# Performance work log

Measured on AMD Instinct MI355X. Metric: run time of the kernel, lower is better.

## Reference

```python
import jax, jax.numpy as jnp
import numpy as np

B, N, E, S, HOPS, OD = 32, 325, 64, 12, 3, 1


def setup_inputs() -> dict:
    key = jax.random.key(0)
    ks = jax.random.split(key, 16)
    rn = lambda k, sh: jax.random.normal(k, sh, dtype=jnp.float32)
    return {
        "hidden": rn(ks[0], (B, N, E)),
        "supports": jax.random.uniform(ks[1], (2, N, N), dtype=jnp.float32),
        "target": rn(ks[2], (B, S, N, OD)),
        "memory": rn(ks[3], (HOPS + 1, B, N, E)),
        "nodevec1": rn(ks[4], (N, E)),
        "nodevec2": rn(ks[5], (N, E)),
        "gru_w_ih": rn(ks[6], (3 * E, OD)) * 0.1,
        "gru_w_hh": rn(ks[7], (3 * E, E)) * 0.1,
        "gru_b_ih": rn(ks[8], (3 * E,)) * 0.1,
        "gru_b_hh": rn(ks[9], (3 * E,)) * 0.1,
        "sent_w": rn(ks[10], (HOPS, E, E)) * 0.1,  # sentinel Linear (no bias), stored pre-transposed
        "bn_gamma": jnp.ones((HOPS, N), dtype=jnp.float32),
        "bn_beta": jnp.zeros((HOPS, N), dtype=jnp.float32),
        "gconv_w": rn(ks[11], (HOPS, 7 * E, E)) * 0.05,  # order*support_len+1 = 7 chunks
        "gconv_b": rn(ks[12], (HOPS, E)) * 0.05,
        "out_w": rn(ks[13], (E, OD)) * 0.1,
        "out_b": rn(ks[14], (OD,)) * 0.1,
    }


def _bn(x, gamma, beta, eps=1e-5):
    # nn.BatchNorm1d(num_nodes) on (B, N, E): channel dim is N, stats over (B, E) (training-mode batch stats)
    mean = x.mean(axis=(0, 2), keepdims=True)
    var = x.var(axis=(0, 2), keepdims=True)
    return (x - mean) / jnp.sqrt(var + eps) * gamma[None, :, None] + beta[None, :, None]


def _gconv(x, sup_list, score, W, b):
    # order=2, support_len=3 -> 1 + 2*3 = 7 concatenated chunks, then Linear(7E -> E)
    outs = [x]
    for adj in sup_list:
        x1 = jnp.einsum('nm,bme->bne', adj, x)
        outs.append(jnp.einsum('bnm,bme->bne', score, x1))
        x2 = jnp.einsum('nm,bme->bne', adj, x1)
        outs.append(jnp.einsum('bnm,bme->bne', score, x2))
    return jnp.concatenate(outs, axis=-1) @ W + b


def reference(hidden, supports, target, memory, nodevec1, nodevec2,
              gru_w_ih, gru_w_hh, gru_b_ih, gru_b_hh, sent_w,
              bn_gamma, bn_beta, gconv_w, gconv_b, out_w, out_b):
    Bn, Nn, Ee = hidden.shape
    scale = Ee ** 0.5
    adp = jax.nn.softmax(jax.nn.relu(nodevec1 @ nodevec2.T), axis=-1)
    sup_list = [supports[0], supports[1], adp]

    def step(carry, _):
        h, prev = carry  # h: (B,N,E), prev: (B,N,OD) previous prediction (zeros at t=0)
        gi = prev.reshape(Bn * Nn, -1) @ gru_w_ih.T + gru_b_ih
        gh = h.reshape(Bn * Nn, Ee) @ gru_w_hh.T + gru_b_hh
        i_r, i_z, i_n = jnp.split(gi, 3, axis=-1)
        h_r, h_z, h_n = jnp.split(gh, 3, axis=-1)
        r = jax.nn.sigmoid(i_r + h_r)
        z = jax.nn.sigmoid(i_z + h_z)
        n = jnp.tanh(i_n + r * h_n)
        h_new = ((1.0 - z) * n + z * h.reshape(Bn * Nn, Ee)).reshape(Bn, Nn, Ee)
        u = h_new
        sents, mems = [], []
        for hop in range(HOPS):
            key_m = memory[hop]  # (B,N,E)
            energy = jnp.einsum('bne,bme->bnm', u, key_m) / scale  # (B,N,N)
            sent = jnp.sum(u * (key_m @ sent_w[hop]), axis=-1) / scale  # (B,N)
            sents.append(sent)
            score = jax.nn.softmax(energy, axis=-1)
            o = _bn(_gconv(memory[hop + 1], sup_list, score, gconv_w[hop], gconv_b[hop]),
                    bn_gamma[hop], bn_beta[hop])
            mems.append(o)
            u = u + o
        sents = jnp.stack(sents, axis=-1)   # (B,N,hops)
        mems = jnp.stack(mems, axis=-2)     # (B,N,hops,E)
        # NOTE: original code weights with RAW sentinel energies, not sentinel_score (dead code) -- kept faithful
        out = jnp.sum(sents[..., None] * mems, axis=-2) @ out_w + out_b  # (B,N,OD)
        return (h_new, out), out

    init_out = jnp.zeros((Bn, Nn, OD), dtype=hidden.dtype)
    _, outs = jax.lax.scan(step, (hidden, init_out), None, length=S)  # (S,B,N,OD)
    return jnp.transpose(outs, (1, 0, 2, 3))  # (B,S,N,OD)
```

## Files before the change

kernel.cpp:

```cpp
#include <hip/hip_runtime.h>

constexpr int B = 32, N = 325, E = 64, S = 12, HOPS = 3;
constexpr int BN  = B * N;
constexpr int BNE = B * N * E;
constexpr int RT  = 16;
constexpr int NRT = (N + RT - 1) / RT;
constexpr int EP  = E + 4;
constexpr int NP  = 328;
constexpr int PBSTR = 360;
constexpr float SCALE_INV = 0.125f;

typedef __attribute__((ext_vector_type(8))) short short8v;
typedef __attribute__((ext_vector_type(4))) float f32x4;

__device__ inline short f2bf(float f) {
  unsigned x = __builtin_bit_cast(unsigned, f);
  return (short)((x + 0x7FFFu + ((x >> 16) & 1u)) >> 16);
}
__device__ inline float bf2f(short h) {
  unsigned x = ((unsigned)(unsigned short)h) << 16;
  return __builtin_bit_cast(float, x);
}

__global__ __launch_bounds__(256) void adp_kernel(const float* __restrict__ nv1,
                                                  const float* __restrict__ nv2,
                                                  float* __restrict__ adp) {
  int n = blockIdx.x;
  __shared__ float row[E];
  __shared__ float buf[N];
  __shared__ float red[256];
  int tid = threadIdx.x;
  if (tid < E) row[tid] = nv1[n * E + tid];
  __syncthreads();
  float lmax = -1e30f;
  for (int m = tid; m < N; m += 256) {
    const float* v2 = nv2 + (size_t)m * E;
    float s = 0.f;
#pragma unroll
    for (int e = 0; e < E; ++e) s += row[e] * v2[e];
    s = fmaxf(s, 0.f);
    buf[m] = s;
    lmax = fmaxf(lmax, s);
  }
  red[tid] = lmax;
  __syncthreads();
  for (int off = 128; off > 0; off >>= 1) {
    if (tid < off) red[tid] = fmaxf(red[tid], red[tid + off]);
    __syncthreads();
  }
  float mx = red[0];
  __syncthreads();
  float lsum = 0.f;
  for (int m = tid; m < N; m += 256) {
    float ev = expf(buf[m] - mx);
    buf[m] = ev;
    lsum += ev;
  }
  red[tid] = lsum;
  __syncthreads();
  for (int off = 128; off > 0; off >>= 1) {
    if (tid < off) red[tid] += red[tid + off];
    __syncthreads();
  }
  float inv = 1.f / red[0];
  for (int m = tid; m < N; m += 256) adp[(size_t)n * N + m] = buf[m] * inv;
}

__device__ inline void rowmm_body(const float* __restrict__ in, const float* __restrict__ W,
                                  const float* __restrict__ bias, float* __restrict__ out,
                                  int accum, int blk, int nblk) {
  __shared__ float Wl[E][E + 1];
  __shared__ float rbuf[4][4][E];
  int tid = threadIdx.x, w = tid >> 6, l = tid & 63;
  for (int idx = tid; idx < E * E; idx += 256) Wl[idx >> 6][idx & 63] = W[idx];
  __syncthreads();
  float bv = bias ? bias[l] : 0.f;
  constexpr int NG = BN / 16;
  for (int g = blk; g < NG; g += nblk) {
    int base = g * 16 + w * 4;
#pragma unroll
    for (int rr = 0; rr < 4; ++rr) rbuf[w][rr][l] = in[(size_t)(base + rr) * E + l];
    float acc[4];
#pragma unroll
    for (int rr = 0; rr < 4; ++rr)
      acc[rr] = accum ? out[(size_t)(base + rr) * E + l] : bv;
#pragma unroll
    for (int k = 0; k < 16; ++k) {
      float w0 = Wl[4 * k][l], w1 = Wl[4 * k + 1][l], w2 = Wl[4 * k + 2][l], w3 = Wl[4 * k + 3][l];
#pragma unroll
      for (int rr = 0; rr < 4; ++rr) {
        float4 rv = *(const float4*)&rbuf[w][rr][4 * k];
        acc[rr] += rv.x * w0 + rv.y * w1 + rv.z * w2 + rv.w * w3;
      }
    }
#pragma unroll
    for (int rr = 0; rr < 4; ++rr) out[(size_t)(base + rr) * E + l] = acc[rr];
  }
}

__global__ __launch_bounds__(256) void rowmmA_kernel(const float* __restrict__ memory,
                                                     const float* __restrict__ sent_w,
                                                     const float* __restrict__ gw,
                                                     const float* __restrict__ gb,
                                                     float* __restrict__ kms,
                                                     float* __restrict__ C0) {
  int c = blockIdx.x / 112, blk = blockIdx.x % 112;
  const float *in, *W, *bias;
  float* out;
  if (c < 3) {
    in = memory + (size_t)c * BNE; W = sent_w + (size_t)c * E * E; bias = nullptr;
    out = kms + (size_t)c * BNE;
  } else {
    int h = c - 3;
    in = memory + (size_t)(h + 1) * BNE; W = gw + (size_t)h * 7 * E * E; bias = gb + h * E;
    out = C0 + (size_t)h * BNE;
  }
  rowmm_body(in, W, bias, out, 0, blk, 112);
}

__global__ __launch_bounds__(256) void rowmmZ_kernel(const float* __restrict__ tbase,
                                                     const float* __restrict__ gw,
                                                     int chunk, float* __restrict__ Zb,
                                                     int accum) {
  int h = blockIdx.x / 224, blk = blockIdx.x % 224;
  rowmm_body(tbase + (size_t)h * BNE, gw + (size_t)h * 7 * E * E + (size_t)chunk * E * E,
             nullptr, Zb + (size_t)h * BNE, accum, blk, 224);
}

__global__ __launch_bounds__(256) void bmmB_kernel(const float* __restrict__ A,
                                                   const float* __restrict__ Xbase,
                                                   float* __restrict__ outBase) {
  int c = blockIdx.x / (B * NRT), rem = blockIdx.x % (B * NRT);
  int b = rem / NRT, rt = rem % NRT;
  const float* X = Xbase + (size_t)c * BNE;
  float* out = outBase + (size_t)c * BNE;
  int n0 = rt * RT, nrows = min(RT, N - n0);
  __shared__ float Ar[RT][NP];
  __shared__ float tile[64][EP];
  int tid = threadIdx.x, w = tid >> 6, l = tid & 63;
  for (int r = w; r < RT; r += 4)
    for (int m = l; m < NP; m += 64)
      Ar[r][m] = (r < nrows && m < N) ? A[(size_t)(n0 + r) * N + m] : 0.f;
  int ti = tid >> 2, c0 = (tid & 3) * 16;
  float acc[4] = {0.f, 0.f, 0.f, 0.f};
  for (int mt = 0; mt < 6; ++mt) {
    int m0 = mt * 64, mv = min(64, N - m0);
    __syncthreads();
    {
      float4 z0, z1, z2, z3;
      if (ti < mv) {
        const float4* src = (const float4*)(X + ((size_t)b * N + m0 + ti) * E + c0);
        z0 = src[0]; z1 = src[1]; z2 = src[2]; z3 = src[3];
      } else {
        z0 = z1 = z2 = z3 = make_float4(0.f, 0.f, 0.f, 0.f);
      }
      float4* dst = (float4*)&tile[ti][c0];
      dst[0] = z0; dst[1] = z1; dst[2] = z2; dst[3] = z3;
    }
    __syncthreads();
    int jmax = (mv + 3) >> 2;
#pragma unroll 4
    for (int j = 0; j < jmax; ++j) {
      float t0 = tile[4 * j][l], t1 = tile[4 * j + 1][l];
      float t2 = tile[4 * j + 2][l], t3 = tile[4 * j + 3][l];
#pragma unroll
      for (int rr = 0; rr < 4; ++rr) {
        float4 p = *(const float4*)&Ar[w * 4 + rr][m0 + 4 * j];
        acc[rr] += p.x * t0 + p.y * t1 + p.z * t2 + p.w * t3;
      }
    }
  }
#pragma unroll
  for (int rr = 0; rr < 4; ++rr) {
    int r = w * 4 + rr;
    if (r < nrows) out[((size_t)b * N + n0 + r) * E + l] = acc[rr];
  }
}

__global__ __launch_bounds__(128) void kpack_kernel(const float* __restrict__ memory,
                                                    short* __restrict__ kp) {
  int idx = blockIdx.x;
  int ct = idx % 21, hb = idx / 21;
  int tid = threadIdx.x, ks = tid >> 6, l = tid & 63;
  int m = ct * 16 + (l & 15);
  int e0 = ks * 32 + (l >> 4) * 8;
  short8v hi, lo;
  if (m < N) {
    const float* p = memory + ((size_t)hb * N + m) * E + e0;
#pragma unroll
    for (int j = 0; j < 8; ++j) {
      float f = p[j];
      short h = f2bf(f);
      hi[j] = h;
      lo[j] = f2bf(f - bf2f(h));
    }
  } else {
#pragma unroll
    for (int j = 0; j < 8; ++j) { hi[j] = 0; lo[j] = 0; }
  }
  size_t base = ((size_t)idx * 2 + ks) * 1024 + (size_t)l * 8;
  *(short8v*)(kp + base) = hi;
  *(short8v*)(kp + base + 512) = lo;
}

__global__ __launch_bounds__(64) void zpack_kernel(const float* __restrict__ Zb,
                                                   short* __restrict__ zp) {
  int idx = blockIdx.x;
  int et = idx & 3, hb = idx >> 2;
  int l = threadIdx.x;
  int e = et * 16 + (l & 15);
  int mbase = (l >> 4) * 8;
  const float* Zp = Zb + (size_t)hb * N * E;
  for (int ks = 0; ks < 11; ++ks) {
    short8v hi, lo;
#pragma unroll
    for (int j = 0; j < 8; ++j) {
      int m = ks * 32 + mbase + j;
      float f = (m < N) ? Zp[(size_t)m * E + e] : 0.f;
      short h = f2bf(f);
      hi[j] = h;
      lo[j] = f2bf(f - bf2f(h));
    }
    size_t base = ((size_t)idx * 11 + ks) * 1024 + (size_t)l * 8;
    *(short8v*)(zp + base) = hi;
    *(short8v*)(zp + base + 512) = lo;
  }
}

__global__ __launch_bounds__(512) void attn_kernel(
    const float* __restrict__ uPrev, const float* __restrict__ gprePrev,
    const float* __restrict__ statsPrev, const float* __restrict__ gammaPrev,
    const float* __restrict__ betaPrev, const float* __restrict__ outw,
    float* __restrict__ uOut, float* __restrict__ owPrev,
    const float* __restrict__ kms, const short* __restrict__ kp,
    const short* __restrict__ zp, const float* __restrict__ C0,
    float* __restrict__ gpre, float* __restrict__ statsCur,
    float* __restrict__ sent) {
  int b = blockIdx.x / 11, rt = blockIdx.x % 11;
  int n0 = rt * 32, nrows = min(32, N - n0);
  int tid = threadIdx.x, w = tid >> 6, l = tid & 63;
  __shared__ float uT[32][68];
  __shared__ short pb[32][PBSTR];
  __shared__ float rowred[32][8];
  __shared__ float rmax[32];
  __shared__ float rsinv[32];
  size_t rowbase = (size_t)b * N + n0;
  int g = l >> 4;

  for (int idx = tid; idx < 32 * (PBSTR - 336); idx += 512) {
    int r = idx / (PBSTR - 336), c = idx - r * (PBSTR - 336);
    pb[r][336 + c] = 0;
  }
#pragma unroll
  for (int rr = 0; rr < 4; ++rr) {
    int r = w * 4 + rr;
    if (r < nrows) {
      size_t gi = (rowbase + r) * E + l;
      float uv;
      if (gprePrev) {
        int n = n0 + r;
        float m = statsPrev[n] * (1.f / 2048.f);
        float var = statsPrev[N + n] * (1.f / 2048.f) - m * m;
        float rstd = rsqrtf(var + 1e-5f);
        float o = (gprePrev[gi] - m) * rstd * gammaPrev[n] + betaPrev[n];
        uv = uPrev[gi] + o;
        if (uOut) uOut[gi] = uv;
        float tt = o * outw[l];
#pragma unroll
        for (int off = 32; off; off >>= 1) tt += __shfl_xor(tt, off);
        if (l == 0) owPrev[rowbase + r] = tt;
      } else {
        uv = uPrev[gi];
      }
      uT[r][l] = uv;
    } else {
      uT[r][l] = 0.f;
    }
  }
  __syncthreads();
#pragma unroll
  for (int rr = 0; rr < 4; ++rr) {
    int r = w * 4 + rr;
    if (r < nrows) {
      float v = uT[r][l] * kms[(rowbase + r) * E + l];
#pragma unroll
      for (int off = 32; off; off >>= 1) v += __shfl_xor(v, off);
      if (l == 0) sent[rowbase + r] = v * SCALE_INV;
    }
  }
  short8v ah[2][2], al[2][2];
  {
    int arow = l & 15, ak = g * 8;
#pragma unroll
    for (int mt = 0; mt < 2; ++mt)
#pragma unroll
      for (int ks = 0; ks < 2; ++ks) {
        const float* p = &uT[mt * 16 + arow][ks * 32 + ak];
        short8v h, lo;
#pragma unroll
        for (int j = 0; j < 8; ++j) {
          float f = p[j];
          short hh = f2bf(f);
          h[j] = hh;
          lo[j] = f2bf(f - bf2f(hh));
        }
        ah[mt][ks] = h; al[mt][ks] = lo;
      }
  }
  const short8v* kpb = (const short8v*)(kp + (size_t)b * 21 * 2048);
  f32x4 acc0[3], acc1[3];
#pragma unroll
  for (int i = 0; i < 3; ++i) {
    acc0[i] = (f32x4){0.f, 0.f, 0.f, 0.f};
    acc1[i] = (f32x4){0.f, 0.f, 0.f, 0.f};
    int ct = w + 8 * i;
    if (ct < 21) {
      short8v bh0 = kpb[(ct * 4 + 0) * 64 + l];
      short8v bl0 = kpb[(ct * 4 + 1) * 64 + l];
      short8v bh1 = kpb[(ct * 4 + 2) * 64 + l];
      short8v bl1 = kpb[(ct * 4 + 3) * 64 + l];
      f32x4 a0 = acc0[i], a1 = acc1[i];
      a0 = __builtin_amdgcn_mfma_f32_16x16x32_bf16(ah[0][0], bh0, a0, 0, 0, 0);
      a0 = __builtin_amdgcn_mfma_f32_16x16x32_bf16(ah[0][0], bl0, a0, 0, 0, 0);
      a0 = __builtin_amdgcn_mfma_f32_16x16x32_bf16(al[0][0], bh0, a0, 0, 0, 0);
      a0 = __builtin_amdgcn_mfma_f32_16x16x32_bf16(ah[0][1], bh1, a0, 0, 0, 0);
      a0 = __builtin_amdgcn_mfma_f32_16x16x32_bf16(ah[0][1], bl1, a0, 0, 0, 0);
      a0 = __builtin_amdgcn_mfma_f32_16x16x32_bf16(al[0][1], bh1, a0, 0, 0, 0);
      a1 = __builtin_amdgcn_mfma_f32_16x16x32_bf16(ah[1][0], bh0, a1, 0, 0, 0);
      a1 = __builtin_amdgcn_mfma_f32_16x16x32_bf16(ah[1][0], bl0, a1, 0, 0, 0);
      a1 = __builtin_amdgcn_mfma_f32_16x16x32_bf16(al[1][0], bh0, a1, 0, 0, 0);
      a1 = __builtin_amdgcn_mfma_f32_16x16x32_bf16(ah[1][1], bh1, a1, 0, 0, 0);
      a1 = __builtin_amdgcn_mfma_f32_16x16x32_bf16(ah[1][1], bl1, a1, 0, 0, 0);
      a1 = __builtin_amdgcn_mfma_f32_16x16x32_bf16(al[1][1], bh1, a1, 0, 0, 0);
      acc0[i] = a0; acc1[i] = a1;
    }
  }
  {
    float m0[4], m1[4];
#pragma unroll
    for (int r = 0; r < 4; ++r) {
      float a = -1e30f, c = -1e30f;
#pragma unroll
      for (int i = 0; i < 3; ++i)
        if (w + 8 * i < 21) { a = fmaxf(a, acc0[i][r]); c = fmaxf(c, acc1[i][r]); }
#pragma unroll
      for (int off = 1; off < 16; off <<= 1) {
        a = fmaxf(a, __shfl_xor(a, off));
        c = fmaxf(c, __shfl_xor(c, off));
      }
      m0[r] = a; m1[r] = c;
    }
    if ((l & 15) == 0) {
#pragma unroll
      for (int r = 0; r < 4; ++r) {
        rowred[g * 4 + r][w] = m0[r];
        rowred[16 + g * 4 + r][w] = m1[r];
      }
    }
  }
  __syncthreads();
  if (tid < 32) {
    float a = rowred[tid][0];
#pragma unroll
    for (int j = 1; j < 8; ++j) a = fmaxf(a, rowred[tid][j]);
    rmax[tid] = a;
  }
  __syncthreads();
  {
    float mx0[4], mx1[4], s0[4], s1[4];
#pragma unroll
    for (int r = 0; r < 4; ++r) {
      mx0[r] = rmax[g * 4 + r]; mx1[r] = rmax[16 + g * 4 + r];
      s0[r] = 0.f; s1[r] = 0.f;
    }
#pragma unroll
    for (int i = 0; i < 3; ++i) {
      int ct = w + 8 * i;
      if (ct < 21) {
        int col = ct * 16 + (l & 15);
        bool valid = col < N;
#pragma unroll
        for (int r = 0; r < 4; ++r) {
          short pv0 = 0, pv1 = 0;
          if (valid) {
            pv0 = f2bf(expf((acc0[i][r] - mx0[r]) * SCALE_INV));
            pv1 = f2bf(expf((acc1[i][r] - mx1[r]) * SCALE_INV));
            s0[r] += bf2f(pv0);
            s1[r] += bf2f(pv1);
          }
          pb[g * 4 + r][col] = pv0;
          pb[16 + g * 4 + r][col] = pv1;
        }
      }
    }
#pragma unroll
    for (int r = 0; r < 4; ++r) {
#pragma unroll
      for (int off = 1; off < 16; off <<= 1) {
        s0[r] += __shfl_xor(s0[r], off);
        s1[r] += __shfl_xor(s1[r], off);
      }
    }
    if ((l & 15) == 0) {
#pragma unroll
      for (int r = 0; r < 4; ++r) {
        rowred[g * 4 + r][w] = s0[r];
        rowred[16 + g * 4 + r][w] = s1[r];
      }
    }
  }
  __syncthreads();
  if (tid < 32) {
    float s = 0.f;
#pragma unroll
    for (int j = 0; j < 8; ++j) s += rowred[tid][j];
    rsinv[tid] = 1.f / s;
  }
  __syncthreads();
  int mt = w >> 2, et = w & 3;
  const short8v* zpb = (const short8v*)(zp + (size_t)b * 4 * 11 * 1024);
  f32x4 acc = {0.f, 0.f, 0.f, 0.f};
  {
    int arow = mt * 16 + (l & 15), ak = g * 8;
#pragma unroll
    for (int ks = 0; ks < 11; ++ks) {
      short8v a = *(const short8v*)&pb[arow][ks * 32 + ak];
      short8v zh = zpb[((et * 11 + ks) * 2 + 0) * 64 + l];
      short8v zl = zpb[((et * 11 + ks) * 2 + 1) * 64 + l];
      acc = __builtin_amdgcn_mfma_f32_16x16x32_bf16(a, zh, acc, 0, 0, 0);
      acc = __builtin_amdgcn_mfma_f32_16x16x32_bf16(a, zl, acc, 0, 0, 0);
    }
  }
  int colA = et * 16 + (l & 15);
#pragma unroll
  for (int r = 0; r < 4; ++r) {
    int row = mt * 16 + g * 4 + r;
    float sval = 0.f, qval = 0.f;
    if (row < nrows) {
      size_t gi = (rowbase + row) * E + colA;
      float gA = acc[r] * rsinv[row] + C0[gi];
      gpre[gi] = gA;
      sval = gA; qval = gA * gA;
    }
#pragma unroll
    for (int off = 1; off < 16; off <<= 1) {
      sval += __shfl_xor(sval, off);
      qval += __shfl_xor(qval, off);
    }
    if ((l & 15) == 0 && row < nrows) {
      atomicAdd(&statsCur[n0 + row], sval);
      atomicAdd(&statsCur[N + n0 + row], qval);
    }
  }
}

__global__ __launch_bounds__(256) void gru_kernel(
    float* __restrict__ h,
    const float* __restrict__ gpre2, const float* __restrict__ stats2,
    const float* __restrict__ gamma2, const float* __restrict__ beta2,
    const float* __restrict__ outw, const float* __restrict__ outb,
    const float* __restrict__ sentb, const float* __restrict__ owb,
    float* __restrict__ dout, int tprev,
    const float* __restrict__ wih, const float* __restrict__ whh,
    const float* __restrict__ bih, const float* __restrict__ bhh,
    float* __restrict__ u) {
  __shared__ float W[3 * E][EP];
  __shared__ float hrow[4][E];
  int tid = threadIdx.x, w = tid >> 6, l = tid & 63;
  for (int idx = tid; idx < 3 * E * E; idx += 256) W[idx >> 6][idx & 63] = whh[idx];
  __syncthreads();
  float wi0 = wih[l], wi1 = wih[64 + l], wi2 = wih[128 + l];
  float bi0 = bih[l], bi1 = bih[64 + l], bi2 = bih[128 + l];
  float bh0 = bhh[l], bh1 = bhh[64 + l], bh2 = bhh[128 + l];
  float wv = outw[l];
  float ob = outb[0];
  int nw = gridDim.x * 4, wid = blockIdx.x * 4 + w;
  for (int row = wid; row < BN; row += nw) {
    float hv = h[(size_t)row * E + l];
    hrow[w][l] = hv;
    float pv = 0.f;
    if (gpre2) {
      int n = row % N;
      float m = stats2[n] * (1.f / 2048.f);
      float var = stats2[N + n] * (1.f / 2048.f) - m * m;
      float rstd = rsqrtf(var + 1e-5f);
      float o = (gpre2[(size_t)row * E + l] - m) * rstd * gamma2[n] + beta2[n];
      float tt = o * wv;
#pragma unroll
      for (int off = 32; off; off >>= 1) tt += __shfl_xor(tt, off);
      float v = ob + sentb[row] * owb[row] + sentb[BN + row] * owb[BN + row]
              + sentb[2 * BN + row] * tt;
      pv = v;
      if (l == 0) {
        int bb = row / N;
        dout[((size_t)bb * S + tprev) * N + (row - bb * N)] = v;
      }
    }
    float g0 = bh0, g1 = bh1, g2 = bh2;
#pragma unroll
    for (int k = 0; k < 16; ++k) {
      float4 hh = *(const float4*)&hrow[w][4 * k];
      float4 a = *(const float4*)&W[l][4 * k];
      float4 bq = *(const float4*)&W[64 + l][4 * k];
      float4 c = *(const float4*)&W[128 + l][4 * k];
      g0 += hh.x * a.x + hh.y * a.y + hh.z * a.z + hh.w * a.w;
      g1 += hh.x * bq.x + hh.y * bq.y + hh.z * bq.z + hh.w * bq.w;
      g2 += hh.x * c.x + hh.y * c.y + hh.z * c.z + hh.w * c.w;
    }
    float i0 = pv * wi0 + bi0;
    float i1 = pv * wi1 + bi1;
    float i2 = pv * wi2 + bi2;
    float r = 1.f / (1.f + expf(-(i0 + g0)));
    float z = 1.f / (1.f + expf(-(i1 + g1)));
    float nn = tanhf(i2 + r * g2);
    float hn = (1.f - z) * nn + z * hv;
    h[(size_t)row * E + l] = hn;
    u[(size_t)row * E + l] = hn;
  }
}

__global__ __launch_bounds__(256) void finish_kernel(
    const float* __restrict__ gpre2, const float* __restrict__ stats2,
    const float* __restrict__ gamma2, const float* __restrict__ beta2,
    const float* __restrict__ outw, const float* __restrict__ outb,
    const float* __restrict__ sent, const float* __restrict__ ow01,
    float* __restrict__ dout, int t) {
  int tid = threadIdx.x, w = tid >> 6, l = tid & 63;
  int wid = blockIdx.x * 4 + w, nw = gridDim.x * 4;
  float wv = outw[l];
  for (int row = wid; row < BN; row += nw) {
    int n = row % N;
    float m = stats2[n] * (1.f / 2048.f);
    float var = stats2[N + n] * (1.f / 2048.f) - m * m;
    float rstd = rsqrtf(var + 1e-5f);
    float o = (gpre2[(size_t)row * E + l] - m) * rstd * gamma2[n] + beta2[n];
    float tt = o * wv;
#pragma unroll
    for (int off = 32; off; off >>= 1) tt += __shfl_xor(tt, off);
    if (l == 0) {
      float v = outb[0] + sent[row] * ow01[row] + sent[BN + row] * ow01[BN + row]
              + sent[2 * BN + row] * tt;
      int b = row / N;
      dout[((size_t)b * S + t) * N + (row - b * N)] = v;
    }
  }
}

extern "C" void kernel_launch(void* const* d_in, const int* in_sizes, int n_in,
                              void* d_out, int out_size, void* d_ws, size_t ws_size,
                              hipStream_t stream) {
  const float* hidden   = (const float*)d_in[0];
  const float* supports = (const float*)d_in[1];
  const float* memory   = (const float*)d_in[3];
  const float* nv1      = (const float*)d_in[4];
  const float* nv2      = (const float*)d_in[5];
  const float* wih      = (const float*)d_in[6];
  const float* whh      = (const float*)d_in[7];
  const float* bih      = (const float*)d_in[8];
  const float* bhh      = (const float*)d_in[9];
  const float* sent_w   = (const float*)d_in[10];
  const float* gamma    = (const float*)d_in[11];
  const float* beta     = (const float*)d_in[12];
  const float* gw       = (const float*)d_in[13];
  const float* gb       = (const float*)d_in[14];
  const float* outw     = (const float*)d_in[15];
  const float* outb     = (const float*)d_in[16];
  float* out = (float*)d_out;
  float* ws  = (float*)d_ws;

  size_t o = 0;
  float* adp   = ws + o; o += 105632;
  float* kms   = ws + o; o += (size_t)3 * BNE;
  float* C0b   = ws + o; o += (size_t)3 * BNE;
  float* hbuf  = ws + o; o += (size_t)BNE;
  float* ubuf  = ws + o; o += (size_t)BNE;
  float* u1    = ws + o; o += (size_t)BNE;
  float* uni   = ws + o; o += (size_t)9 * BNE;
  float* Zb  = uni;
  float* t1b = uni + (size_t)3 * BNE;
  float* t2b = uni + (size_t)6 * BNE;
  float* g0 = uni, *g1 = uni + BNE, *g2 = uni + (size_t)2 * BNE;
  short* kpackS = (short*)(ws + o); o += 2064384;
  short* zpackS = (short*)(ws + o); o += 2162688;
  float* sentb  = ws + o; o += (size_t)3 * BN;
  float* owb    = ws + o; o += (size_t)2 * BN;
  float* statsb = ws + o; o += (size_t)36 * 650;

  hipMemcpyAsync(hbuf, hidden, sizeof(float) * BNE, hipMemcpyDeviceToDevice, stream);
  hipMemsetAsync(statsb, 0, sizeof(float) * 36 * 650, stream);

  adp_kernel<<<N, 256, 0, stream>>>(nv1, nv2, adp);
  rowmmA_kernel<<<672, 256, 0, stream>>>(memory, sent_w, gw, gb, kms, C0b);
  kpack_kernel<<<3 * B * 21, 128, 0, stream>>>(memory, kpackS);

  for (int a = 0; a < 3; ++a) {
    const float* A = (a == 0) ? supports : (a == 1) ? supports + (size_t)N * N : adp;
    bmmB_kernel<<<3 * B * NRT, 256, 0, stream>>>(A, memory + BNE, t1b);
    rowmmZ_kernel<<<672, 256, 0, stream>>>(t1b, gw, 2 * a + 1, Zb, (a > 0) ? 1 : 0);
    bmmB_kernel<<<3 * B * NRT, 256, 0, stream>>>(A, t1b, t2b);
    rowmmZ_kernel<<<672, 256, 0, stream>>>(t2b, gw, 2 * a + 2, Zb, 1);
  }
  zpack_kernel<<<3 * B * 4, 64, 0, stream>>>(Zb, zpackS);

  for (int t = 0; t < S; ++t) {
    float* st0 = statsb + (size_t)(t * 3 + 0) * 650;
    float* st1 = statsb + (size_t)(t * 3 + 1) * 650;
    float* st2 = statsb + (size_t)(t * 3 + 2) * 650;
    const float* g2prev  = (t == 0) ? nullptr : g2;
    const float* st2prev = (t == 0) ? nullptr : statsb + (size_t)((t - 1) * 3 + 2) * 650;
    gru_kernel<<<512, 256, 0, stream>>>(hbuf, g2prev, st2prev, gamma + 2 * N, beta + 2 * N,
                                        outw, outb, sentb, owb, out, t - 1,
                                        wih, whh, bih, bhh, ubuf);
    attn_kernel<<<B * 11, 512, 0, stream>>>(
        ubuf, nullptr, nullptr, nullptr, nullptr, outw, nullptr, nullptr,
        kms, kpackS, zpackS, C0b, g0, st0, sentb);
    attn_kernel<<<B * 11, 512, 0, stream>>>(
        ubuf, g0, st0, gamma, beta, outw, u1, owb,
        kms + BNE, kpackS + (size_t)B * 21 * 2048, zpackS + (size_t)B * 4 * 11 * 1024,
        C0b + BNE, g1, st1, sentb + BN);
    attn_kernel<<<B * 11, 512, 0, stream>>>(
        u1, g1, st1, gamma + N, beta + N, outw, nullptr, owb + BN,
        kms + (size_t)2 * BNE, kpackS + (size_t)2 * B * 21 * 2048,
        zpackS + (size_t)2 * B * 4 * 11 * 1024,
        C0b + (size_t)2 * BNE, g2, st2, sentb + (size_t)2 * BN);
  }
  finish_kernel<<<256, 256, 0, stream>>>(g2, statsb + (size_t)(11 * 3 + 2) * 650,
                                         gamma + 2 * N, beta + 2 * N,
                                         outw, outb, sentb, owb, out, S - 1);
}
```

Measured before the change: 2.304 ms.

## Replace FP32 support-matrix bmm with split-bf16 MFMA kernel and packed operands

Swaps the scalar FP32 adjacency-by-activation batched matmul (bmmB) for an MFMA-based kernel that uses three bf16 hi/lo products to approximate FP32 accuracy. The support matrices and activations are pre-packed into MFMA fragment layout by new apack and zpack launches, so the inner loop is plain fragment loads plus MFMAs. This targets the heavy scalar FMA and LDS cost of the graph-diffusion precompute. In exchange it adds packing kernels and workspace buffers, and the dropped lo×lo term loses a little precision.

```diff
diff --git a/kernel.cpp b/kernel.cpp
--- a/kernel.cpp
+++ b/kernel.cpp
@@ -3,10 +3,7 @@
 constexpr int B = 32, N = 325, E = 64, S = 12, HOPS = 3;
 constexpr int BN  = B * N;
 constexpr int BNE = B * N * E;
-constexpr int RT  = 16;
-constexpr int NRT = (N + RT - 1) / RT;
 constexpr int EP  = E + 4;
-constexpr int NP  = 328;
 constexpr int PBSTR = 360;
 constexpr float SCALE_INV = 0.125f;
 
@@ -127,54 +124,79 @@
              nullptr, Zb + (size_t)h * BNE, accum, blk, 224);
 }
 
-__global__ __launch_bounds__(256) void bmmB_kernel(const float* __restrict__ A,
-                                                   const float* __restrict__ Xbase,
-                                                   float* __restrict__ outBase) {
-  int c = blockIdx.x / (B * NRT), rem = blockIdx.x % (B * NRT);
-  int b = rem / NRT, rt = rem % NRT;
-  const float* X = Xbase + (size_t)c * BNE;
-  float* out = outBase + (size_t)c * BNE;
-  int n0 = rt * RT, nrows = min(RT, N - n0);
-  __shared__ float Ar[RT][NP];
-  __shared__ float tile[64][EP];
+__global__ __launch_bounds__(64) void apack_kernel(const float* __restrict__ supports,
+                                                   const float* __restrict__ adp,
+                                                   short* __restrict__ ap) {
+  int blk = blockIdx.x;
+  int nt = blk % 21, a = blk / 21;
+  const float* A = (a < 2) ? supports + (size_t)a * N * N : adp;
+  int l = threadIdx.x;
+  int row = nt * 16 + (l & 15);
+  int k0 = (l >> 4) * 8;
+  for (int ks = 0; ks < 11; ++ks) {
+    short8v hi, lo;
+#pragma unroll
+    for (int j = 0; j < 8; ++j) {
+      int m = ks * 32 + k0 + j;
+      float f = (row < N && m < N) ? A[(size_t)row * N + m] : 0.f;
+      short h = f2bf(f);
+      hi[j] = h;
+      lo[j] = f2bf(f - bf2f(h));
+    }
+    size_t base = ((size_t)(blk * 11 + ks) * 2) * 512 + (size_t)l * 8;
+    *(short8v*)(ap + base) = hi;
+    *(short8v*)(ap + base + 512) = lo;
+  }
+}
+
+__global__ __launch_bounds__(64) void zpack_kernel(const float* __restrict__ Zb,
+                                                   short* __restrict__ zp) {
+  int idx = blockIdx.x;
+  int et = idx & 3, hb = idx >> 2;
+  int l = threadIdx.x;
+  int e = et * 16 + (l & 15);
+  int mbase = (l >> 4) * 8;
+  const float* Zp = Zb + (size_t)hb * N * E;
+  for (int ks = 0; ks < 11; ++ks) {
+    short8v hi, lo;
+#pragma unroll
+    for (int j = 0; j < 8; ++j) {
+      int m = ks * 32 + mbase + j;
+      float f = (m < N) ? Zp[(size_t)m * E + e] : 0.f;
+      short h = f2bf(f);
+      hi[j] = h;
+      lo[j] = f2bf(f - bf2f(h));
+    }
+    size_t base = ((size_t)idx * 11 + ks) * 1024 + (size_t)l * 8;
+    *(short8v*)(zp + base) = hi;
+    *(short8v*)(zp + base + 512) = lo;
+  }
+}
+
+__global__ __launch_bounds__(256) void bmmM_kernel(const short* __restrict__ ap,
+                                                   const short* __restrict__ xp,
+                                                   float* __restrict__ out) {
+  int blk = blockIdx.x;
+  int nt = blk % 21, hb = blk / 21;
   int tid = threadIdx.x, w = tid >> 6, l = tid & 63;
-  for (int r = w; r < RT; r += 4)
-    for (int m = l; m < NP; m += 64)
-      Ar[r][m] = (r < nrows && m < N) ? A[(size_t)(n0 + r) * N + m] : 0.f;
-  int ti = tid >> 2, c0 = (tid & 3) * 16;
-  float acc[4] = {0.f, 0.f, 0.f, 0.f};
-  for (int mt = 0; mt < 6; ++mt) {
-    int m0 = mt * 64, mv = min(64, N - m0);
-    __syncthreads();
-    {
-      float4 z0, z1, z2, z3;
-      if (ti < mv) {
-        const float4* src = (const float4*)(X + ((size_t)b * N + m0 + ti) * E + c0);
-        z0 = src[0]; z1 = src[1]; z2 = src[2]; z3 = src[3];
-      } else {
-        z0 = z1 = z2 = z3 = make_float4(0.f, 0.f, 0.f, 0.f);
-      }
-      float4* dst = (float4*)&tile[ti][c0];
-      dst[0] = z0; dst[1] = z1; dst[2] = z2; dst[3] = z3;
-    }
-    __syncthreads();
-    int jmax = (mv + 3) >> 2;
-#pragma unroll 4
-    for (int j = 0; j < jmax; ++j) {
-      float t0 = tile[4 * j][l], t1 = tile[4 * j + 1][l];
-      float t2 = tile[4 * j + 2][l], t3 = tile[4 * j + 3][l];
-#pragma unroll
-      for (int rr = 0; rr < 4; ++rr) {
-        float4 p = *(const float4*)&Ar[w * 4 + rr][m0 + 4 * j];
-        acc[rr] += p.x * t0 + p.y * t1 + p.z * t2 + p.w * t3;
-      }
-    }
-  }
-#pragma unroll
-  for (int rr = 0; rr < 4; ++rr) {
-    int r = w * 4 + rr;
-    if (r < nrows) out[((size_t)b * N + n0 + r) * E + l] = acc[rr];
-  }
+  const short8v* apf = (const short8v*)ap;
+  const short8v* xpf = (const short8v*)(xp + (((size_t)hb * 4 + w) * 11) * 1024);
+  f32x4 acc = {0.f, 0.f, 0.f, 0.f};
+#pragma unroll
+  for (int ks = 0; ks < 11; ++ks) {
+    short8v ah = apf[((nt * 11 + ks) * 2 + 0) * 64 + l];
+    short8v al = apf[((nt * 11 + ks) * 2 + 1) * 64 + l];
+    short8v xh = xpf[(ks * 2 + 0) * 64 + l];
+    short8v xl = xpf[(ks * 2 + 1) * 64 + l];
+    acc = __builtin_amdgcn_mfma_f32_16x16x32_bf16(ah, xh, acc, 0, 0, 0);
+    acc = __builtin_amdgcn_mfma_f32_16x16x32_bf16(ah, xl, acc, 0, 0, 0);
+    acc = __builtin_amdgcn_mfma_f32_16x16x32_bf16(al, xh, acc, 0, 0, 0);
+  }
+  int row = nt * 16 + (l >> 4) * 4, col = w * 16 + (l & 15);
+  float* o = out + (size_t)hb * N * E;
+#pragma unroll
+  for (int r = 0; r < 4; ++r)
+    if (row + r < N) o[(size_t)(row + r) * E + col] = acc[r];
 }
 
 __global__ __launch_bounds__(128) void kpack_kernel(const float* __restrict__ memory,
@@ -201,30 +223,6 @@
   size_t base = ((size_t)idx * 2 + ks) * 1024 + (size_t)l * 8;
   *(short8v*)(kp + base) = hi;
   *(short8v*)(kp + base + 512) = lo;
-}
-
-__global__ __launch_bounds__(64) void zpack_kernel(const float* __restrict__ Zb,
-                                                   short* __restrict__ zp) {
-  int idx = blockIdx.x;
-  int et = idx & 3, hb = idx >> 2;
-  int l = threadIdx.x;
-  int e = et * 16 + (l & 15);
-  int mbase = (l >> 4) * 8;
-  const float* Zp = Zb + (size_t)hb * N * E;
-  for (int ks = 0; ks < 11; ++ks) {
-    short8v hi, lo;
-#pragma unroll
-    for (int j = 0; j < 8; ++j) {
-      int m = ks * 32 + mbase + j;
-      float f = (m < N) ? Zp[(size_t)m * E + e] : 0.f;
-      short h = f2bf(f);
-      hi[j] = h;
-      lo[j] = f2bf(f - bf2f(h));
-    }
-    size_t base = ((size_t)idx * 11 + ks) * 1024 + (size_t)l * 8;
-    *(short8v*)(zp + base) = hi;
-    *(short8v*)(zp + base + 512) = lo;
-  }
 }
 
 __global__ __launch_bounds__(512) void attn_kernel(
@@ -582,6 +580,9 @@
   float* g0 = uni, *g1 = uni + BNE, *g2 = uni + (size_t)2 * BNE;
   short* kpackS = (short*)(ws + o); o += 2064384;
   short* zpackS = (short*)(ws + o); o += 2162688;
+  short* apackS = (short*)(ws + o); o += 354816;
+  short* xp0    = (short*)(ws + o); o += 2162688;
+  short* xp1    = (short*)(ws + o); o += 2162688;
   float* sentb  = ws + o; o += (size_t)3 * BN;
   float* owb    = ws + o; o += (size_t)2 * BN;
   float* statsb = ws + o; o += (size_t)36 * 650;
@@ -592,12 +593,15 @@
   adp_kernel<<<N, 256, 0, stream>>>(nv1, nv2, adp);
   rowmmA_kernel<<<672, 256, 0, stream>>>(memory, sent_w, gw, gb, kms, C0b);
   kpack_kernel<<<3 * B * 21, 128, 0, stream>>>(memory, kpackS);
+  apack_kernel<<<63, 64, 0, stream>>>(supports, adp, apackS);
+  zpack_kernel<<<3 * B * 4, 64, 0, stream>>>(memory + BNE, xp0);
 
   for (int a = 0; a < 3; ++a) {
-    const float* A = (a == 0) ? supports : (a == 1) ? supports + (size_t)N * N : adp;
-    bmmB_kernel<<<3 * B * NRT, 256, 0, stream>>>(A, memory + BNE, t1b);
+    const short* apA = apackS + (size_t)a * 21 * 11 * 2 * 512;
+    bmmM_kernel<<<96 * 21, 256, 0, stream>>>(apA, xp0, t1b);
     rowmmZ_kernel<<<672, 256, 0, stream>>>(t1b, gw, 2 * a + 1, Zb, (a > 0) ? 1 : 0);
-    bmmB_kernel<<<3 * B * NRT, 256, 0, stream>>>(A, t1b, t2b);
+    zpack_kernel<<<3 * B * 4, 64, 0, stream>>>(t1b, xp1);
+    bmmM_kernel<<<96 * 21, 256, 0, stream>>>(apA, xp1, t2b);
     rowmmZ_kernel<<<672, 256, 0, stream>>>(t2b, gw, 2 * a + 2, Zb, 1);
   }
   zpack_kernel<<<3 * B * 4, 64, 0, stream>>>(Zb, zpackS);
```

New measurement: 2.097 ms. 1.1x faster.
